# Optimization experiments

Measured on AMD Instinct MI355X. Metric: run time of the kernel, lower is better.

Reference implementation:

```python
import jax, jax.numpy as jnp
import numpy as np

N = 50000
E = 1600000
NEG_SLOPE = 0.2
BN_EPS = 1e-5


def gat_conv(x, src, dst, W, a_s, a_d, b):
    """PyG-style GATConv (concat=True). a_s/a_d: [H, C]."""
    H, C = a_s.shape
    h = (x @ W).reshape(-1, H, C)  # [N, H, C]
    alpha_src = jnp.einsum('nhc,hc->nh', h, a_s)  # [N, H]
    alpha_dst = jnp.einsum('nhc,hc->nh', h, a_d)  # [N, H]
    e = jax.nn.leaky_relu(alpha_src[src] + alpha_dst[dst], NEG_SLOPE)  # [E, H]
    # segment softmax over edges sharing the same destination node
    m = jax.ops.segment_max(e, dst, num_segments=N)
    e = jnp.exp(e - m[dst])
    s = jax.ops.segment_sum(e, dst, num_segments=N)
    alpha = e / (s[dst] + 1e-16)  # [E, H]
    msg = h[src] * alpha[:, :, None]  # [E, H, C]
    out = jax.ops.segment_sum(msg, dst, num_segments=N)  # [N, H, C]
    return out.reshape(-1, H * C) + b


def batch_norm(x, g, beta):
    mu = jnp.mean(x, axis=0)
    var = jnp.var(x, axis=0)
    return (x - mu) * jax.lax.rsqrt(var + BN_EPS) * g + beta


def setup_inputs() -> dict:
    key = jax.random.key(0)
    ks = jax.random.split(key, 20)
    d_in, hid, heads, d_out = 128, 16, 4, 40
    hh = hid * heads  # 64
    inp = {
        'x': jax.random.normal(ks[0], (N, d_in), jnp.float32),
        'edge_index': jax.random.randint(ks[1], (2, E), 0, N, jnp.int32),
        # layer 0: in -> hid*heads
        'W0': jax.random.normal(ks[2], (d_in, hh), jnp.float32) * 0.05,
        'a_src0': jax.random.normal(ks[3], (heads, hid), jnp.float32) * 0.05,
        'a_dst0': jax.random.normal(ks[4], (heads, hid), jnp.float32) * 0.05,
        'b0': jnp.zeros((hh,), jnp.float32),
        'g0': jnp.ones((hh,), jnp.float32),
        'beta0': jnp.zeros((hh,), jnp.float32),
        # layer 1: hid*heads -> hid*heads
        'W1': jax.random.normal(ks[5], (hh, hh), jnp.float32) * 0.1,
        'a_src1': jax.random.normal(ks[6], (heads, hid), jnp.float32) * 0.1,
        'a_dst1': jax.random.normal(ks[7], (heads, hid), jnp.float32) * 0.1,
        'b1': jnp.zeros((hh,), jnp.float32),
        'g1': jnp.ones((hh,), jnp.float32),
        'beta1': jnp.zeros((hh,), jnp.float32),
        # layer 2: hid*heads -> out, heads=1
        'W2': jax.random.normal(ks[8], (hh, d_out), jnp.float32) * 0.1,
        'a_src2': jax.random.normal(ks[9], (1, d_out), jnp.float32) * 0.1,
        'a_dst2': jax.random.normal(ks[10], (1, d_out), jnp.float32) * 0.1,
        'b2': jnp.zeros((d_out,), jnp.float32),
    }
    return inp


def reference(x, edge_index, W0, a_src0, a_dst0, b0, g0, beta0,
              W1, a_src1, a_dst1, b1, g1, beta1,
              W2, a_src2, a_dst2, b2):
    # add self-loops (PyG GATConv default)
    loop = jnp.arange(N, dtype=edge_index.dtype)
    src = jnp.concatenate([edge_index[0], loop])
    dst = jnp.concatenate([edge_index[1], loop])

    h = gat_conv(x, src, dst, W0, a_src0, a_dst0, b0)
    h = jax.nn.relu(batch_norm(h, g0, beta0))
    h = gat_conv(h, src, dst, W1, a_src1, a_dst1, b1)
    h = jax.nn.relu(batch_norm(h, g1, beta1))
    h = gat_conv(h, src, dst, W2, a_src2, a_dst2, b2)
    return jax.nn.log_softmax(h, axis=-1)
```

## Files before the change

kernel.cpp:

```cpp
#include <hip/hip_runtime.h>
#include <math.h>

#define NEG_SLOPE 0.2f
#define CAP 128
#define BCAP 6144

__device__ __forceinline__ unsigned enc_f(float f) {
    unsigned b = __float_as_uint(f);
    return (b & 0x80000000u) ? ~b : (b | 0x80000000u);
}
__device__ __forceinline__ float dec_f(unsigned u) {
    return (u & 0x80000000u) ? __uint_as_float(u ^ 0x80000000u) : __uint_as_float(~u);
}
#define ENC_NEG_INF 0x007FFFFFu

__device__ __forceinline__ unsigned short f2bf(float f) {
    unsigned u = __float_as_uint(f);
    u += 0x7fffu + ((u >> 16) & 1u);
    return (unsigned short)(u >> 16);
}
__device__ __forceinline__ float bf2f(unsigned short b) {
    return __uint_as_float(((unsigned)b) << 16);
}

static inline int nblk(long total, int b) { return (int)((total + b - 1) / b); }

__global__ void init_kernel(int* bincnt, float* bn, unsigned* menc, int nbin) {
    int i = blockIdx.x * blockDim.x + threadIdx.x;
    if (i < nbin) bincnt[i] = 0;
    if (i < 256) bn[i] = 0.f;
    if (i < 16) menc[i] = ENC_NEG_INF;
}

__global__ void bin_kernel(const int* __restrict__ srcs, const int* __restrict__ dsts,
                           int E_, int EA, int nbin, int* bincnt, unsigned* __restrict__ binbuf) {
    __shared__ int lh[512];
    __shared__ int lbase[512];
    int tid = threadIdx.x;
    for (int i = tid; i < nbin; i += 256) lh[i] = 0;
    __syncthreads();
    int chunk = (EA + gridDim.x - 1) / gridDim.x;
    int e0 = blockIdx.x * chunk;
    int e1 = e0 + chunk; if (e1 > EA) e1 = EA;
    for (int i = e0 + tid; i < e1; i += 256) {
        int d = (i < E_) ? dsts[i] : (i - E_);
        atomicAdd(&lh[d >> 7], 1);
    }
    __syncthreads();
    for (int i = tid; i < nbin; i += 256) {
        lbase[i] = atomicAdd(&bincnt[i], lh[i]);
        lh[i] = 0;
    }
    __syncthreads();
    for (int i = e0 + tid; i < e1; i += 256) {
        int s, d;
        if (i < E_) { s = srcs[i]; d = dsts[i]; } else { s = d = i - E_; }
        int b = d >> 7;
        int pos = lbase[b] + atomicAdd(&lh[b], 1);
        if (pos < BCAP) binbuf[(size_t)b * BCAP + pos] = ((unsigned)s << 16) | (unsigned)d;
    }
}

__global__ void build_kernel(const unsigned* __restrict__ binbuf, const int* __restrict__ bincnt,
                             unsigned short* __restrict__ esrc, int* __restrict__ cnt, int n) {
    __shared__ unsigned short slab[128 * CAP];
    __shared__ int lcnt[128];
    int tid = threadIdx.x;
    int b = blockIdx.x, d0 = b << 7;
    if (tid < 128) lcnt[tid] = 0;
    __syncthreads();
    int nb = bincnt[b]; if (nb > BCAP) nb = BCAP;
    for (int i = tid; i < nb; i += 256) {
        unsigned u = binbuf[(size_t)b * BCAP + i];
        int s = (int)(u >> 16);
        int ld = (int)(u & 0xffffu) - d0;
        int pos = atomicAdd(&lcnt[ld], 1);
        if (pos < CAP) slab[ld * CAP + pos] = (unsigned short)s;
    }
    __syncthreads();
    const uint4* sl = (const uint4*)slab;
    uint4* outp = (uint4*)esrc;
    for (int i = tid; i < 128 * CAP / 8; i += 256) {
        int r = i >> 4;
        if (d0 + r < n) outp[(size_t)(d0 + r) * (CAP / 8) + (i & 15)] = sl[i];
    }
    if (tid < 128 && d0 + tid < n) cnt[d0 + tid] = lcnt[tid];
}

template <int K, bool BN>
__global__ __launch_bounds__(256) void gemm_alpha_kernel(
    const float* __restrict__ X, const float* __restrict__ W,
    const float* __restrict__ a_s, const float* __restrict__ a_d,
    unsigned short* __restrict__ Hout, float* __restrict__ as_o,
    float* __restrict__ ad_o, unsigned* menc_, int n,
    const float* __restrict__ bnsum, const float* __restrict__ bnsq,
    const float* __restrict__ g, const float* __restrict__ beta) {
    __shared__ float Xs[32][132];
    __shared__ float Ws[32][64];
    __shared__ float scale[BN ? K : 4];
    __shared__ float shift[BN ? K : 4];
    __shared__ float redm[4][4];

    int tid = threadIdx.x;
    if (BN) {
        if (tid < K) {
            float inv_n = 1.0f / (float)n;
            float mu = bnsum[tid] * inv_n;
            float var = bnsq[tid] * inv_n - mu * mu;
            float sc = rsqrtf(var + 1e-5f) * g[tid];
            scale[tid] = sc;
            shift[tid] = beta[tid] - mu * sc;
        }
        __syncthreads();
    }

    int node0 = blockIdx.x * 128;
    int tx = tid & 7;
    int ty = tid >> 3;

    int snode = tid & 127;
    int khalf = (tid >> 7) * 16;
    int src_row = node0 + snode; if (src_row >= n) src_row = n - 1;
    const float* xrow = X + (size_t)src_row * K;

    float acc[4][8];
#pragma unroll
    for (int i = 0; i < 4; ++i)
#pragma unroll
        for (int j = 0; j < 8; ++j) acc[i][j] = 0.f;

    constexpr int NCH = K / 32;
    for (int c = 0; c < NCH; ++c) {
        int k0 = c * 32;
#pragma unroll
        for (int r = 0; r < 2; ++r) {
            int f = tid + r * 256;
            int kk = f >> 4;
            int cq = f & 15;
            float4 wv4 = *(const float4*)(W + (size_t)(k0 + kk) * 64 + cq * 4);
            *(float4*)&Ws[kk][cq * 4] = wv4;
        }
#pragma unroll
        for (int q = 0; q < 4; ++q) {
            int kk = khalf + q * 4;
            float4 v = *(const float4*)(xrow + k0 + kk);
            if (BN) {
                float4 sc = *(const float4*)(&scale[k0 + kk]);
                float4 sh = *(const float4*)(&shift[k0 + kk]);
                v.x = fmaxf(fmaf(v.x, sc.x, sh.x), 0.f);
                v.y = fmaxf(fmaf(v.y, sc.y, sh.y), 0.f);
                v.z = fmaxf(fmaf(v.z, sc.z, sh.z), 0.f);
                v.w = fmaxf(fmaf(v.w, sc.w, sh.w), 0.f);
            }
            Xs[kk + 0][snode] = v.x;
            Xs[kk + 1][snode] = v.y;
            Xs[kk + 2][snode] = v.z;
            Xs[kk + 3][snode] = v.w;
        }
        __syncthreads();
#pragma unroll 2
        for (int kk = 0; kk < 32; ++kk) {
            float4 xv = *(const float4*)(&Xs[kk][ty * 4]);
            float4 wa = *(const float4*)(&Ws[kk][tx * 8]);
            float4 wb = *(const float4*)(&Ws[kk][tx * 8 + 4]);
            float xs_[4] = {xv.x, xv.y, xv.z, xv.w};
            float ws_[8] = {wa.x, wa.y, wa.z, wa.w, wb.x, wb.y, wb.z, wb.w};
#pragma unroll
            for (int i = 0; i < 4; ++i)
#pragma unroll
                for (int j = 0; j < 8; ++j)
                    acc[i][j] = fmaf(xs_[i], ws_[j], acc[i][j]);
        }
        __syncthreads();
    }

    float4 asa = *(const float4*)(a_s + tx * 8);
    float4 asb = *(const float4*)(a_s + tx * 8 + 4);
    float4 ada = *(const float4*)(a_d + tx * 8);
    float4 adb = *(const float4*)(a_d + tx * 8 + 4);
    int head = tx >> 1;
    float p1v[4], p2v[4];
#pragma unroll
    for (int i = 0; i < 4; ++i) {
        float p1 = acc[i][0] * asa.x + acc[i][1] * asa.y + acc[i][2] * asa.z + acc[i][3] * asa.w
                 + acc[i][4] * asb.x + acc[i][5] * asb.y + acc[i][6] * asb.z + acc[i][7] * asb.w;
        float p2 = acc[i][0] * ada.x + acc[i][1] * ada.y + acc[i][2] * ada.z + acc[i][3] * ada.w
                 + acc[i][4] * adb.x + acc[i][5] * adb.y + acc[i][6] * adb.z + acc[i][7] * adb.w;
        p1 += __shfl_xor(p1, 1, 64);
        p2 += __shfl_xor(p2, 1, 64);
        p1v[i] = p1; p2v[i] = p2;
    }
#pragma unroll
    for (int i = 0; i < 4; ++i) {
        int node = node0 + ty * 4 + i;
        if (node < n) {
            unsigned r0 = (unsigned)f2bf(acc[i][0]) | ((unsigned)f2bf(acc[i][1]) << 16);
            unsigned r1 = (unsigned)f2bf(acc[i][2]) | ((unsigned)f2bf(acc[i][3]) << 16);
            unsigned r2 = (unsigned)f2bf(acc[i][4]) | ((unsigned)f2bf(acc[i][5]) << 16);
            unsigned r3 = (unsigned)f2bf(acc[i][6]) | ((unsigned)f2bf(acc[i][7]) << 16);
            *(uint4*)(Hout + (size_t)node * 64 + tx * 8) = make_uint4(r0, r1, r2, r3);
            if ((tx & 1) == 0) {
                as_o[(size_t)node * 4 + head] = p1v[i];
                ad_o[(size_t)node * 4 + head] = p2v[i];
            }
        }
    }
    float am = -1e30f;
    if ((tx & 1) == 0)
        am = fmaxf(fmaxf(p1v[0], p1v[1]), fmaxf(p1v[2], p1v[3]));
    am = fmaxf(am, __shfl_xor(am, 8, 64));
    am = fmaxf(am, __shfl_xor(am, 16, 64));
    am = fmaxf(am, __shfl_xor(am, 32, 64));
    int lane = tid & 63;
    if (lane < 8 && (lane & 1) == 0) redm[tid >> 6][lane >> 1] = am;
    __syncthreads();
    if (tid < 4) {
        float m = fmaxf(fmaxf(redm[0][tid], redm[1][tid]), fmaxf(redm[2][tid], redm[3][tid]));
        atomicMax(&menc_[tid], enc_f(m));
    }
}

__global__ void gather64_kernel(const int* __restrict__ cnt,
                                const unsigned short* __restrict__ esrc,
                                const float* __restrict__ as_, const float* __restrict__ ad_,
                                const unsigned short* __restrict__ Hf,
                                const unsigned* __restrict__ menc,
                                const float* __restrict__ bias, float* __restrict__ feat, int n) {
    int tid = threadIdx.x;
    int wv = tid >> 6, lane = tid & 63;
    int slot = lane >> 4, ql = lane & 15, hq = ql >> 2;
    int node = blockIdx.x * 4 + wv;
    if (node >= n) return;

    int deg = cnt[node]; if (deg > CAP) deg = CAP;
    const unsigned short* ep = esrc + (size_t)node * CAP;
    float4 adv = *(const float4*)(ad_ + (size_t)node * 4);
    float adh = (slot == 0) ? adv.x : (slot == 1) ? adv.y : (slot == 2) ? adv.z : adv.w;
    float mm = dec_f(menc[slot]) + adh;
    float mh = mm > 0.f ? mm : NEG_SLOPE * mm;

    float4 acc = make_float4(0.f, 0.f, 0.f, 0.f);
    float wp = 0.f;
    for (int base = 0; base < deg; base += 16) {
        int lim = deg - base; if (lim > 16) lim = 16;
        int s = 0; float w = 0.f;
        if (ql < lim) {
            s = (int)ep[base + ql];
            float ev = as_[(size_t)s * 4 + slot] + adh;
            ev = ev > 0.f ? ev : NEG_SLOPE * ev;
            w = __expf(ev - mh);
        }
        wp += w;
#pragma unroll
        for (int i = 0; i < 4; ++i) {
            if (i * 4 >= lim) break;
            int cj = i * 4 + slot;
            int sj = __shfl(s, cj, 64);
            float wj = __shfl(w, hq * 16 + cj, 64);
            ushort4 hv = *(const ushort4*)(Hf + (size_t)sj * 64 + ql * 4);
            acc.x = fmaf(bf2f(hv.x), wj, acc.x);
            acc.y = fmaf(bf2f(hv.y), wj, acc.y);
            acc.z = fmaf(bf2f(hv.z), wj, acc.z);
            acc.w = fmaf(bf2f(hv.w), wj, acc.w);
        }
    }
#pragma unroll
    for (int o = 16; o < 64; o <<= 1) {
        acc.x += __shfl_xor(acc.x, o, 64);
        acc.y += __shfl_xor(acc.y, o, 64);
        acc.z += __shfl_xor(acc.z, o, 64);
        acc.w += __shfl_xor(acc.w, o, 64);
    }
#pragma unroll
    for (int o = 1; o < 16; o <<= 1) wp += __shfl_xor(wp, o, 64);
    float wsh = __shfl(wp, hq << 4, 64);
    if (slot == 0) {
        float inv = 1.0f / (wsh + 1e-16f);
        float4 bv = *(const float4*)(bias + ql * 4);
        float4 rr;
        rr.x = fmaf(acc.x, inv, bv.x);
        rr.y = fmaf(acc.y, inv, bv.y);
        rr.z = fmaf(acc.z, inv, bv.z);
        rr.w = fmaf(acc.w, inv, bv.w);
        *(float4*)(feat + (size_t)node * 64 + ql * 4) = rr;
    }
}

__global__ void prep2_kernel(const float* __restrict__ feat, const float* __restrict__ bnsum,
                             const float* __restrict__ bnsq, const float* __restrict__ g,
                             const float* __restrict__ beta, const float* __restrict__ W2,
                             const float* __restrict__ as2v, const float* __restrict__ ad2v,
                             unsigned short* __restrict__ z, float* __restrict__ as_o,
                             float* __restrict__ ad_o, unsigned* menc_, int n) {
    __shared__ float sc[64], sh[64], vs[64], vd[64];
    int tid = threadIdx.x;
    if (tid < 64) {
        float inv_n = 1.0f / (float)n;
        float mu = bnsum[tid] * inv_n;
        float var = bnsq[tid] * inv_n - mu * mu;
        float s = rsqrtf(var + 1e-5f) * g[tid];
        sc[tid] = s;
        sh[tid] = beta[tid] - mu * s;
    } else if (tid < 128) {
        int k = tid - 64;
        float s1 = 0.f, s2 = 0.f;
        for (int j = 0; j < 40; ++j) {
            float wv = W2[k * 40 + j];
            s1 = fmaf(wv, as2v[j], s1);
            s2 = fmaf(wv, ad2v[j], s2);
        }
        vs[k] = s1;
        vd[k] = s2;
    }
    __syncthreads();
    int lane = tid & 63, wv = tid >> 6;
    float scl = sc[lane], shl = sh[lane], vsl = vs[lane], vdl = vd[lane];
    float amax = -1e30f;
    int nwaves = gridDim.x * 4;
    for (int node = blockIdx.x * 4 + wv; node < n; node += nwaves) {
        float v = fmaf(feat[(size_t)node * 64 + lane], scl, shl);
        v = v > 0.f ? v : 0.f;
        z[(size_t)node * 64 + lane] = f2bf(v);
        float p1 = v * vsl, p2 = v * vdl;
#pragma unroll
        for (int o = 1; o < 64; o <<= 1) {
            p1 += __shfl_xor(p1, o, 64);
            p2 += __shfl_xor(p2, o, 64);
        }
        amax = fmaxf(amax, p1);
        if (lane == 0) { as_o[node] = p1; ad_o[node] = p2; }
    }
    if (lane == 0) atomicMax(menc_, enc_f(amax));
}

__global__ void gatherz_kernel(const int* __restrict__ cnt,
                               const unsigned short* __restrict__ esrc,
                               const float* __restrict__ as_, const float* __restrict__ ad_,
                               const unsigned short* __restrict__ Z,
                               const unsigned* __restrict__ menc,
                               float* __restrict__ agg, int n) {
    int tid = threadIdx.x;
    int wv = tid >> 6, lane = tid & 63;
    int slot = lane >> 4, ql = lane & 15;
    int node = blockIdx.x * 4 + wv;
    if (node >= n) return;

    int deg = cnt[node]; if (deg > CAP) deg = CAP;
    const unsigned short* ep = esrc + (size_t)node * CAP;
    float adv = ad_[node];
    float mm = dec_f(menc[0]) + adv;
    float mh = mm > 0.f ? mm : NEG_SLOPE * mm;

    float4 acc = make_float4(0.f, 0.f, 0.f, 0.f);
    float wp = 0.f;
    for (int base = 0; base < deg; base += 64) {
        int lim = deg - base; if (lim > 64) lim = 64;
        int s = 0; float w = 0.f;
        if (lane < lim) {
            s = (int)ep[base + lane];
            float ev = as_[s] + adv;
            ev = ev > 0.f ? ev : NEG_SLOPE * ev;
            w = __expf(ev - mh);
        }
        wp += w;
#pragma unroll
        for (int i = 0; i < 16; ++i) {
            if (i * 4 >= lim) break;
            int cj = i * 4 + slot;
            int sj = __shfl(s, cj, 64);
            float wj = __shfl(w, cj, 64);
            ushort4 hv = *(const ushort4*)(Z + (size_t)sj * 64 + ql * 4);
            acc.x = fmaf(bf2f(hv.x), wj, acc.x);
            acc.y = fmaf(bf2f(hv.y), wj, acc.y);
            acc.z = fmaf(bf2f(hv.z), wj, acc.z);
            acc.w = fmaf(bf2f(hv.w), wj, acc.w);
        }
    }
#pragma unroll
    for (int o = 16; o < 64; o <<= 1) {
        acc.x += __shfl_xor(acc.x, o, 64);
        acc.y += __shfl_xor(acc.y, o, 64);
        acc.z += __shfl_xor(acc.z, o, 64);
        acc.w += __shfl_xor(acc.w, o, 64);
    }
#pragma unroll
    for (int o = 1; o < 64; o <<= 1) wp += __shfl_xor(wp, o, 64);
    if (slot == 0) {
        float inv = 1.0f / (wp + 1e-16f);
        float4 rr;
        rr.x = acc.x * inv;
        rr.y = acc.y * inv;
        rr.z = acc.z * inv;
        rr.w = acc.w * inv;
        *(float4*)(agg + (size_t)node * 64 + ql * 4) = rr;
    }
}

__global__ __launch_bounds__(64) void gemm_lsm_kernel(const float* __restrict__ X,
                                                      const float* __restrict__ W,
                                                      const float* __restrict__ bias,
                                                      float* __restrict__ out, int n) {
    constexpr int K = 64, M = 40;
    int lane = threadIdx.x;
    int node = blockIdx.x * 64 + lane;
    int nodec = node < n ? node : n - 1;
    const float* xp = X + (size_t)nodec * K;

    float4 xr[16];
#pragma unroll
    for (int q = 0; q < 16; ++q) xr[q] = *(const float4*)(xp + q * 4);

    float4 wq[2][10];
#pragma unroll
    for (int rr = 0; rr < 2; ++rr)
#pragma unroll
        for (int q = 0; q < 10; ++q)
            wq[rr][q] = *(const float4*)(W + rr * M + q * 4);

    float acc[M];
#pragma unroll
    for (int c = 0; c < M; ++c) acc[c] = 0.f;

    for (int jb = 0; jb < K; jb += 2) {
#pragma unroll
        for (int jj = 0; jj < 2; ++jj) {
            int j = jb + jj;
            float4 xq4 = xr[j >> 2];
            int jm = j & 3;
            float xs = jm == 0 ? xq4.x : jm == 1 ? xq4.y : jm == 2 ? xq4.z : xq4.w;
            float4 w_[10];
#pragma unroll
            for (int q = 0; q < 10; ++q) w_[q] = wq[jj][q];
            int jn = j + 2; jn = jn < K ? jn : K - 1;
            const float* wr = W + (size_t)jn * M;
#pragma unroll
            for (int q = 0; q < 10; ++q) wq[jj][q] = *(const float4*)(wr + q * 4);
#pragma unroll
            for (int q = 0; q < 10; ++q) {
                acc[q * 4 + 0] = fmaf(xs, w_[q].x, acc[q * 4 + 0]);
                acc[q * 4 + 1] = fmaf(xs, w_[q].y, acc[q * 4 + 1]);
                acc[q * 4 + 2] = fmaf(xs, w_[q].z, acc[q * 4 + 2]);
                acc[q * 4 + 3] = fmaf(xs, w_[q].w, acc[q * 4 + 3]);
            }
        }
    }

    float m2 = -1e30f;
#pragma unroll
    for (int c = 0; c < M; ++c) {
        acc[c] += bias[c];
        m2 = fmaxf(m2, acc[c]);
    }
    float ex = 0.f;
#pragma unroll
    for (int c = 0; c < M; ++c) ex += __expf(acc[c] - m2);
    float ls = m2 + logf(ex);
    if (node < n) {
        float4* op = (float4*)(out + (size_t)node * M);
#pragma unroll
        for (int q = 0; q < M / 4; ++q) {
            float4 rr;
            rr.x = acc[q * 4 + 0] - ls;
            rr.y = acc[q * 4 + 1] - ls;
            rr.z = acc[q * 4 + 2] - ls;
            rr.w = acc[q * 4 + 3] - ls;
            op[q] = rr;
        }
    }
}

__global__ void bn_stats_kernel(const float* __restrict__ feat, float* bnsum, float* bnsq,
                                int n) {
    __shared__ float ls[256], lq[256];
    int f = threadIdx.x & 63, y = threadIdx.x >> 6;
    float ps = 0.f, pq = 0.f;
    for (int node = blockIdx.x * 4 + y; node < n; node += gridDim.x * 4) {
        float v = feat[(size_t)node * 64 + f];
        ps += v;
        pq += v * v;
    }
    ls[threadIdx.x] = ps;
    lq[threadIdx.x] = pq;
    __syncthreads();
    if (y == 0) {
        atomicAdd(&bnsum[f], ls[f] + ls[f + 64] + ls[f + 128] + ls[f + 192]);
        atomicAdd(&bnsq[f], lq[f] + lq[f + 64] + lq[f + 128] + lq[f + 192]);
    }
}

extern "C" void kernel_launch(void* const* d_in, const int* in_sizes, int n_in,
                              void* d_out, int out_size, void* d_ws, size_t ws_size,
                              hipStream_t stream) {
    const float* x   = (const float*)d_in[0];
    const int*   ei  = (const int*)d_in[1];
    const float* W0  = (const float*)d_in[2];
    const float* as0 = (const float*)d_in[3];
    const float* ad0 = (const float*)d_in[4];
    const float* b0  = (const float*)d_in[5];
    const float* g0  = (const float*)d_in[6];
    const float* be0 = (const float*)d_in[7];
    const float* W1  = (const float*)d_in[8];
    const float* as1 = (const float*)d_in[9];
    const float* ad1 = (const float*)d_in[10];
    const float* b1  = (const float*)d_in[11];
    const float* g1  = (const float*)d_in[12];
    const float* be1 = (const float*)d_in[13];
    const float* W2  = (const float*)d_in[14];
    const float* as2 = (const float*)d_in[15];
    const float* ad2 = (const float*)d_in[16];
    const float* b2  = (const float*)d_in[17];

    const int N  = in_sizes[0] / 128;
    const int E  = in_sizes[1] / 2;
    const int EA = E + N;
    const int NBIN = (N + 127) >> 7;
    const int* srcs = ei;
    const int* dsts = ei + E;

    float* ws    = (float*)d_ws;
    float* feat  = ws;
    float* agg   = feat + (size_t)N * 64;
    float* asrc  = agg + (size_t)N * 64;
    float* adst  = asrc + (size_t)N * 4;
    float* bn    = adst + (size_t)N * 4;
    unsigned* menc = (unsigned*)(bn + 256);
    int* bincnt  = (int*)(menc + 16);
    int* cnt     = bincnt + 512;
    unsigned short* hb   = (unsigned short*)(cnt + N);
    unsigned short* esrc = hb + (size_t)N * 64;
    unsigned* binbuf = (unsigned*)(esrc + (size_t)N * CAP);

    float* bn0sum = bn, *bn0sq = bn + 64, *bn1sum = bn + 128, *bn1sq = bn + 192;

    init_kernel<<<2, 256, 0, stream>>>(bincnt, bn, menc, NBIN);
    bin_kernel<<<512, 256, 0, stream>>>(srcs, dsts, E, EA, NBIN, bincnt, binbuf);
    build_kernel<<<NBIN, 256, 0, stream>>>(binbuf, bincnt, esrc, cnt, N);

    gemm_alpha_kernel<128, false><<<nblk(N, 128), 256, 0, stream>>>(
        x, W0, as0, ad0, hb, asrc, adst, menc, N, nullptr, nullptr, nullptr, nullptr);
    gather64_kernel<<<nblk(N, 4), 256, 0, stream>>>(cnt, esrc, asrc, adst, hb, menc, b0, feat, N);
    bn_stats_kernel<<<512, 256, 0, stream>>>(feat, bn0sum, bn0sq, N);

    gemm_alpha_kernel<64, true><<<nblk(N, 128), 256, 0, stream>>>(
        feat, W1, as1, ad1, hb, asrc, adst, menc + 4, N, bn0sum, bn0sq, g0, be0);
    gather64_kernel<<<nblk(N, 4), 256, 0, stream>>>(cnt, esrc, asrc, adst, hb, menc + 4, b1,
                                                    feat, N);
    bn_stats_kernel<<<512, 256, 0, stream>>>(feat, bn1sum, bn1sq, N);

    prep2_kernel<<<512, 256, 0, stream>>>(feat, bn1sum, bn1sq, g1, be1, W2, as2, ad2,
                                          hb, asrc, adst, menc + 8, N);
    gatherz_kernel<<<nblk(N, 4), 256, 0, stream>>>(cnt, esrc, asrc, adst, hb, menc + 8, agg, N);
    gemm_lsm_kernel<<<nblk(N, 64), 64, 0, stream>>>(agg, W2, b2, (float*)d_out, N);
}
```

Measured before the change: 442.1 us.

## Software-pipeline gather index loads and tile final GEMM+log-softmax via shared memory

In gather64_kernel, the neighbor indices and source attention scores for upcoming 16-edge chunks are prefetched one or two chunks ahead, so that dependent global loads overlap with the accumulation. The final GEMM+log_softmax kernel is rewritten from one-thread-per-node with 64-thread blocks into a 256-thread, 128-node tile that stages X and W in LDS. Each thread computes a 4x5 output tile, and the row max and sum are reduced across 8 lanes with shuffles. This cuts per-thread register pressure and repeated W loads, but adds extra registers for the prefetch and two barriers per K-chunk.

```diff
diff --git a/kernel.cpp b/kernel.cpp
--- a/kernel.cpp
+++ b/kernel.cpp
@@ -241,16 +241,31 @@
 
     float4 acc = make_float4(0.f, 0.f, 0.f, 0.f);
     float wp = 0.f;
-    for (int base = 0; base < deg; base += 16) {
-        int lim = deg - base; if (lim > 16) lim = 16;
-        int s = 0; float w = 0.f;
-        if (ql < lim) {
-            s = (int)ep[base + ql];
-            float ev = as_[(size_t)s * 4 + slot] + adh;
-            ev = ev > 0.f ? ev : NEG_SLOPE * ev;
-            w = __expf(ev - mh);
+    int nch = (deg + 15) >> 4;
+
+    int lim0 = deg < 16 ? deg : 16;
+    int sP = (ql < lim0) ? (int)ep[ql] : 0;
+    float asv = as_[(size_t)sP * 4 + slot];
+    int sN = 0;
+    if (nch > 1) {
+        int lim1 = deg - 16; if (lim1 > 16) lim1 = 16;
+        sN = (ql < lim1) ? (int)ep[16 + ql] : 0;
+    }
+
+    for (int c = 0; c < nch; ++c) {
+        int lim = deg - c * 16; if (lim > 16) lim = 16;
+        float ev = asv + adh;
+        ev = ev > 0.f ? ev : NEG_SLOPE * ev;
+        float w = (ql < lim) ? __expf(ev - mh) : 0.f;
+        float asvN = 0.f;
+        if (c + 1 < nch) asvN = as_[(size_t)sN * 4 + slot];
+        int sNN = 0;
+        if (c + 2 < nch) {
+            int l2 = deg - (c + 2) * 16; if (l2 > 16) l2 = 16;
+            sNN = (ql < l2) ? (int)ep[(c + 2) * 16 + ql] : 0;
         }
         wp += w;
+        int s = sP;
 #pragma unroll
         for (int i = 0; i < 4; ++i) {
             if (i * 4 >= lim) break;
@@ -263,6 +278,7 @@
             acc.z = fmaf(bf2f(hv.z), wj, acc.z);
             acc.w = fmaf(bf2f(hv.w), wj, acc.w);
         }
+        sP = sN; sN = sNN; asv = asvN;
     }
 #pragma unroll
     for (int o = 16; o < 64; o <<= 1) {
@@ -396,75 +412,91 @@
     }
 }
 
-__global__ __launch_bounds__(64) void gemm_lsm_kernel(const float* __restrict__ X,
-                                                      const float* __restrict__ W,
-                                                      const float* __restrict__ bias,
-                                                      float* __restrict__ out, int n) {
-    constexpr int K = 64, M = 40;
-    int lane = threadIdx.x;
-    int node = blockIdx.x * 64 + lane;
-    int nodec = node < n ? node : n - 1;
-    const float* xp = X + (size_t)nodec * K;
-
-    float4 xr[16];
-#pragma unroll
-    for (int q = 0; q < 16; ++q) xr[q] = *(const float4*)(xp + q * 4);
-
-    float4 wq[2][10];
-#pragma unroll
-    for (int rr = 0; rr < 2; ++rr)
-#pragma unroll
-        for (int q = 0; q < 10; ++q)
-            wq[rr][q] = *(const float4*)(W + rr * M + q * 4);
-
-    float acc[M];
-#pragma unroll
-    for (int c = 0; c < M; ++c) acc[c] = 0.f;
-
-    for (int jb = 0; jb < K; jb += 2) {
-#pragma unroll
-        for (int jj = 0; jj < 2; ++jj) {
-            int j = jb + jj;
-            float4 xq4 = xr[j >> 2];
-            int jm = j & 3;
-            float xs = jm == 0 ? xq4.x : jm == 1 ? xq4.y : jm == 2 ? xq4.z : xq4.w;
-            float4 w_[10];
-#pragma unroll
-            for (int q = 0; q < 10; ++q) w_[q] = wq[jj][q];
-            int jn = j + 2; jn = jn < K ? jn : K - 1;
-            const float* wr = W + (size_t)jn * M;
-#pragma unroll
-            for (int q = 0; q < 10; ++q) wq[jj][q] = *(const float4*)(wr + q * 4);
-#pragma unroll
-            for (int q = 0; q < 10; ++q) {
-                acc[q * 4 + 0] = fmaf(xs, w_[q].x, acc[q * 4 + 0]);
-                acc[q * 4 + 1] = fmaf(xs, w_[q].y, acc[q * 4 + 1]);
-                acc[q * 4 + 2] = fmaf(xs, w_[q].z, acc[q * 4 + 2]);
-                acc[q * 4 + 3] = fmaf(xs, w_[q].w, acc[q * 4 + 3]);
+__global__ __launch_bounds__(256) void gemm_lsm_kernel(const float* __restrict__ X,
+                                                       const float* __restrict__ W,
+                                                       const float* __restrict__ bias,
+                                                       float* __restrict__ out, int n) {
+    __shared__ float Xs[32][132];
+    __shared__ float Ws[32][40];
+    __shared__ float bs[40];
+    int tid = threadIdx.x;
+    if (tid < 40) bs[tid] = bias[tid];
+
+    int node0 = blockIdx.x * 128;
+    int tx = tid & 7;
+    int ty = tid >> 3;
+    int snode = tid & 127;
+    int khalf = (tid >> 7) * 16;
+    int src_row = node0 + snode; if (src_row >= n) src_row = n - 1;
+    const float* xrow = X + (size_t)src_row * 64;
+
+    float acc[4][5];
+#pragma unroll
+    for (int i = 0; i < 4; ++i)
+#pragma unroll
+        for (int j = 0; j < 5; ++j) acc[i][j] = 0.f;
+
+    for (int c = 0; c < 2; ++c) {
+        int k0 = c * 32;
+        for (int f = tid; f < 320; f += 256) {
+            int kk = f / 10, q = f - kk * 10;
+            *(float4*)&Ws[kk][q * 4] = *(const float4*)(W + (size_t)(k0 + kk) * 40 + q * 4);
+        }
+#pragma unroll
+        for (int q = 0; q < 4; ++q) {
+            int kk = khalf + q * 4;
+            float4 v = *(const float4*)(xrow + k0 + kk);
+            Xs[kk + 0][snode] = v.x;
+            Xs[kk + 1][snode] = v.y;
+            Xs[kk + 2][snode] = v.z;
+            Xs[kk + 3][snode] = v.w;
+        }
+        __syncthreads();
+#pragma unroll 2
+        for (int kk = 0; kk < 32; ++kk) {
+            float4 xv = *(const float4*)(&Xs[kk][ty * 4]);
+            float w0 = Ws[kk][tx * 5 + 0];
+            float w1 = Ws[kk][tx * 5 + 1];
+            float w2 = Ws[kk][tx * 5 + 2];
+            float w3 = Ws[kk][tx * 5 + 3];
+            float w4 = Ws[kk][tx * 5 + 4];
+            float xs_[4] = {xv.x, xv.y, xv.z, xv.w};
+#pragma unroll
+            for (int i = 0; i < 4; ++i) {
+                acc[i][0] = fmaf(xs_[i], w0, acc[i][0]);
+                acc[i][1] = fmaf(xs_[i], w1, acc[i][1]);
+                acc[i][2] = fmaf(xs_[i], w2, acc[i][2]);
+                acc[i][3] = fmaf(xs_[i], w3, acc[i][3]);
+                acc[i][4] = fmaf(xs_[i], w4, acc[i][4]);
             }
         }
-    }
-
-    float m2 = -1e30f;
-#pragma unroll
-    for (int c = 0; c < M; ++c) {
-        acc[c] += bias[c];
-        m2 = fmaxf(m2, acc[c]);
-    }
-    float ex = 0.f;
-#pragma unroll
-    for (int c = 0; c < M; ++c) ex += __expf(acc[c] - m2);
-    float ls = m2 + logf(ex);
-    if (node < n) {
-        float4* op = (float4*)(out + (size_t)node * M);
-#pragma unroll
-        for (int q = 0; q < M / 4; ++q) {
-            float4 rr;
-            rr.x = acc[q * 4 + 0] - ls;
-            rr.y = acc[q * 4 + 1] - ls;
-            rr.z = acc[q * 4 + 2] - ls;
-            rr.w = acc[q * 4 + 3] - ls;
-            op[q] = rr;
+        __syncthreads();
+    }
+
+    float b0 = bs[tx * 5 + 0], b1 = bs[tx * 5 + 1], b2 = bs[tx * 5 + 2],
+          b3 = bs[tx * 5 + 3], b4 = bs[tx * 5 + 4];
+#pragma unroll
+    for (int i = 0; i < 4; ++i) {
+        float v0 = acc[i][0] + b0, v1 = acc[i][1] + b1, v2 = acc[i][2] + b2,
+              v3 = acc[i][3] + b3, v4 = acc[i][4] + b4;
+        float m = fmaxf(fmaxf(fmaxf(v0, v1), fmaxf(v2, v3)), v4);
+        m = fmaxf(m, __shfl_xor(m, 1, 64));
+        m = fmaxf(m, __shfl_xor(m, 2, 64));
+        m = fmaxf(m, __shfl_xor(m, 4, 64));
+        float ex = __expf(v0 - m) + __expf(v1 - m) + __expf(v2 - m)
+                 + __expf(v3 - m) + __expf(v4 - m);
+        ex += __shfl_xor(ex, 1, 64);
+        ex += __shfl_xor(ex, 2, 64);
+        ex += __shfl_xor(ex, 4, 64);
+        float ls = m + logf(ex);
+        int node = node0 + ty * 4 + i;
+        if (node < n) {
+            float* op = out + (size_t)node * 40 + tx * 5;
+            op[0] = v0 - ls;
+            op[1] = v1 - ls;
+            op[2] = v2 - ls;
+            op[3] = v3 - ls;
+            op[4] = v4 - ls;
         }
     }
 }
@@ -550,5 +582,5 @@
     prep2_kernel<<<512, 256, 0, stream>>>(feat, bn1sum, bn1sq, g1, be1, W2, as2, ad2,
                                           hb, asrc, adst, menc + 8, N);
     gatherz_kernel<<<nblk(N, 4), 256, 0, stream>>>(cnt, esrc, asrc, adst, hb, menc + 8, agg, N);
-    gemm_lsm_kernel<<<nblk(N, 64), 64, 0, stream>>>(agg, W2, b2, (float*)d_out, N);
-}
+    gemm_lsm_kernel<<<nblk(N, 128), 256, 0, stream>>>(agg, W2, b2, (float*)d_out, N);
+}
```

Result: faster. 401.7 us (-9.1%).
